# Kernel optimization log

Hardware: AMD Instinct MI355X
Metric: run time of the kernel (lower is better)

The kernel has to match this reference:

```python
import jax, jax.numpy as jnp
import numpy as np
from jax import lax

B, N, C = 16, 1024, 768
HID = 128           # route_hidden_dim (Cattn bottleneck + router hidden)
OUT = 2304          # qkv out_feature


def setup_inputs() -> dict:
    key = jax.random.key(0)
    ks = jax.random.split(key, 16)
    s = 0.02
    return {
        "input":  jax.random.normal(ks[0], (B, N, C), jnp.float32),
        "H": 32,
        "W": 32,
        "input2": jax.random.normal(ks[1], (B, N, C), jnp.float32),
        # qkv linear
        "qkv_w": jax.random.normal(ks[2], (OUT, C), jnp.float32) * s,
        "qkv_b": jax.random.normal(ks[3], (OUT,), jnp.float32) * s,
        # Cattn (vida_refine): fc1 -> dwconv -> gelu -> fc2
        "fc1_w": jax.random.normal(ks[4], (HID, C), jnp.float32) * s,
        "fc1_b": jnp.zeros((HID,), jnp.float32),
        "dw_w":  jax.random.normal(ks[5], (HID, 1, 3, 3), jnp.float32) * np.sqrt(2.0 / 9.0),
        "dw_b":  jnp.zeros((HID,), jnp.float32),
        "fc2_w": jax.random.normal(ks[6], (C, HID), jnp.float32) * s,
        "fc2_b": jnp.zeros((C,), jnp.float32),
        # router MLP: 1 -> HID -> 2
        "r1_w": jax.random.normal(ks[7], (HID, 1), jnp.float32) * s,
        "r1_b": jnp.zeros((HID,), jnp.float32),
        "r2_w": jax.random.normal(ks[8], (2, HID), jnp.float32) * s,
        "r2_b": jnp.zeros((2,), jnp.float32),
    }


def _linear(x, w, b):
    return jnp.einsum("bnc,oc->bno", x, w) + b


def _cattn(x, H, W, fc1_w, fc1_b, dw_w, dw_b, fc2_w, fc2_b):
    # fc1 -> depthwise 3x3 conv over HxW -> GELU(exact) -> fc2
    x = _linear(x, fc1_w, fc1_b)                       # [B,N,HID]
    b, n, h = x.shape
    xi = x.transpose(0, 2, 1).reshape(b, h, H, W)      # [B,HID,H,W]
    xi = lax.conv_general_dilated(
        xi, dw_w, window_strides=(1, 1), padding="SAME",
        feature_group_count=h,
        dimension_numbers=("NCHW", "OIHW", "NCHW"),
    ) + dw_b[None, :, None, None]
    x = xi.reshape(b, h, n).transpose(0, 2, 1)         # [B,N,HID]
    x = jax.nn.gelu(x, approximate=False)              # torch nn.GELU default = erf
    return _linear(x, fc2_w, fc2_b)                    # [B,N,C]


def _get_logit(inp, refine_x2):
    # cosine sim between per-batch token-mean of `inp` and refine_x2, then
    # per-batch min-max normalization (skipped when max == min)
    mean = jnp.mean(inp, axis=1, keepdims=True)        # [B,1,C]
    dot = jnp.sum(refine_x2 * mean, axis=-1, keepdims=True)
    n1 = jnp.linalg.norm(mean, axis=-1, keepdims=True)
    n2 = jnp.linalg.norm(refine_x2, axis=-1, keepdims=True)
    csim = dot / (n1 * n2)                             # [B,N,1]
    mn = jnp.min(csim, axis=1, keepdims=True)
    mx = jnp.max(csim, axis=1, keepdims=True)
    rng = mx - mn
    return jnp.where(rng != 0, (csim - mn) / jnp.where(rng != 0, rng, 1.0), csim)


def reference(input, H, W, input2, qkv_w, qkv_b, fc1_w, fc1_b, dw_w, dw_b,
              fc2_w, fc2_b, r1_w, r1_b, r2_w, r2_b):
    q1 = _linear(input, qkv_w, qkv_b)                              # [B,N,OUT]
    refine_x2 = input2 + _cattn(input2, H, W, fc1_w, fc1_b, dw_w, dw_b, fc2_w, fc2_b)
    q2 = _linear(refine_x2, qkv_w, qkv_b)                          # [B,N,OUT]
    csim = _get_logit(input, refine_x2)                            # [B,N,1]
    h = jax.nn.relu(_linear(csim, r1_w, r1_b))                     # [B,N,HID]
    logits = jax.nn.sigmoid(_linear(h, r2_w, r2_b))                # [B,N,2]
    # gumbel_softmax(hard=False, tau=1) with a fixed key for determinism
    g = jax.random.gumbel(jax.random.key(42), logits.shape, logits.dtype)
    router = jax.nn.softmax(logits + g, axis=-1)[:, :, 0]          # [B,N]
    return (q1, q2, router)
```

## Files before the change

### kernel.cpp

```cpp
#include <hip/hip_runtime.h>
#include <cstdint>
#include <cstddef>

#define BQ 16
#define NT 1024
#define CH 768
#define HIDN 128
#define OUTF 2304
#define MTOT (BQ*NT)

typedef __attribute__((ext_vector_type(4))) float f32x4;
typedef __attribute__((ext_vector_type(8))) short short8;

__device__ __forceinline__ unsigned short f2bf(float f){
  unsigned u = __float_as_uint(f);
  u += 0x7FFFu + ((u >> 16) & 1u);
  return (unsigned short)(u >> 16);
}
__device__ __forceinline__ float bf2f(unsigned short h){
  return __uint_as_float(((unsigned)h) << 16);
}

__device__ __forceinline__ void gload16(const void* g, void* l){
  __builtin_amdgcn_global_load_lds((const __attribute__((address_space(1))) void*)g,
                                   (__attribute__((address_space(3))) void*)l, 16, 0, 0);
}

__device__ __forceinline__ void mfma16(f32x4& d, short8 a, short8 b){
  asm volatile("v_mfma_f32_16x16x32_bf16 %0, %1, %2, %0" : "+v"(d) : "v"(a), "v"(b));
}

__global__ void k_f2bf_all(const float* __restrict__ in0, const float* __restrict__ in1,
                           const float* __restrict__ in2, const float* __restrict__ in3,
                           const float* __restrict__ in4,
                           unsigned short* __restrict__ o0, unsigned short* __restrict__ o1,
                           unsigned short* __restrict__ o2, unsigned short* __restrict__ o3,
                           unsigned short* __restrict__ o4)
{
  const long step = (long)2048 * 256 * 4;
  for (long i = (long)(blockIdx.x * 256 + threadIdx.x) * 4; i < 27131904L; i += step){
    const float* s; unsigned short* d; long off;
    if      (i < 12582912L){ s = in0; d = o0; off = i; }
    else if (i < 25165824L){ s = in1; d = o1; off = i - 12582912L; }
    else if (i < 26935296L){ s = in2; d = o2; off = i - 25165824L; }
    else if (i < 27033600L){ s = in3; d = o3; off = i - 26935296L; }
    else                   { s = in4; d = o4; off = i - 27033600L; }
    float4 v = *reinterpret_cast<const float4*>(s + off);
    ushort4 o;
    o.x = f2bf(v.x); o.y = f2bf(v.y); o.z = f2bf(v.z); o.w = f2bf(v.w);
    *reinterpret_cast<ushort4*>(d + off) = o;
  }
}

__global__ void k_mean(const unsigned short* __restrict__ x1b, float* __restrict__ meanb,
                       float* __restrict__ n1p){
  const int b = blockIdx.x, cg = blockIdx.y;
  const int tid = threadIdx.x;
  const int oct = tid & 15, rg = tid >> 4;
  const unsigned short* ip = x1b + (size_t)b*NT*CH + (size_t)rg*64*CH + cg*128 + oct*8;

  float s[8];
  #pragma unroll
  for (int j = 0; j < 8; ++j) s[j] = 0.f;
  #pragma unroll 4
  for (int r = 0; r < 64; ++r){
    short8 v = *reinterpret_cast<const short8*>(ip + (size_t)r*CH);
    #pragma unroll
    for (int j = 0; j < 8; ++j) s[j] += bf2f((unsigned short)v[j]);
  }

  __shared__ float tmp[16][128];
  #pragma unroll
  for (int j = 0; j < 8; ++j) tmp[rg][oct*8 + j] = s[j];
  __syncthreads();

  if (tid < 128){
    float m = 0.f;
    #pragma unroll
    for (int g = 0; g < 16; ++g) m += tmp[g][tid];
    m *= (1.0f/1024.0f);
    meanb[b*CH + cg*128 + tid] = m;
    float q = m * m;
    for (int off = 32; off; off >>= 1) q += __shfl_down(q, off, 64);
    if ((tid & 63) == 0) n1p[b*12 + cg*2 + (tid >> 6)] = q;
  }
}

template<int EPI>
__global__ __launch_bounds__(256, 2)
void k_gemm(const unsigned short* __restrict__ A, const unsigned short* __restrict__ B,
            const float* __restrict__ bias, const unsigned short* __restrict__ addb,
            unsigned short* __restrict__ Cb,
            const float* __restrict__ meanb, float* __restrict__ part,
            int M, int N, int K)
{
  __shared__ unsigned short sA[128][32];
  __shared__ unsigned short sB[128][32];
  const int tid = threadIdx.x;
  const int wv = tid >> 6, ln = tid & 63;
  const int wr = wv >> 1, wc = wv & 1;
  const int lhi = ln >> 4, llo = ln & 15;
  const int m0 = blockIdx.x * 128, n0 = blockIdx.y * 128;

  f32x4 acc[4][4];
  #pragma unroll
  for (int m = 0; m < 4; ++m)
    #pragma unroll
    for (int n = 0; n < 4; ++n) acc[m][n] = 0.0f;

  const int lrow = ln >> 2;
  const int lk8  = (ln & 3) * 8;

  for (int kt = 0; kt < K; kt += 32){
    #pragma unroll
    for (int cc = 0; cc < 2; ++cc){
      int c = wv * 2 + cc;
      gload16(A + (size_t)(m0 + c*16 + lrow) * K + kt + lk8, &sA[c*16][0]);
      gload16(B + (size_t)(n0 + c*16 + lrow) * K + kt + lk8, &sB[c*16][0]);
    }
    __syncthreads();

    short8 av[4], bv[4];
    #pragma unroll
    for (int m = 0; m < 4; ++m)
      av[m] = *reinterpret_cast<const short8*>(&sA[wr*64 + m*16 + llo][lhi*8]);
    #pragma unroll
    for (int n = 0; n < 4; ++n)
      bv[n] = *reinterpret_cast<const short8*>(&sB[wc*64 + n*16 + llo][lhi*8]);

    #pragma unroll
    for (int m = 0; m < 4; ++m)
      #pragma unroll
      for (int n = 0; n < 4; ++n)
        mfma16(acc[m][n], bv[n], av[m]);
    __syncthreads();
  }

  asm volatile("s_nop 7\n\ts_nop 7\n\ts_nop 7" ::: );

  float4 bias4[4];
  #pragma unroll
  for (int n = 0; n < 4; ++n)
    bias4[n] = *reinterpret_cast<const float4*>(&bias[n0 + wc*64 + n*16 + lhi*4]);

  if (EPI == 0){
    #pragma unroll
    for (int m = 0; m < 4; ++m){
      const int row = m0 + wr*64 + m*16 + llo;
      #pragma unroll
      for (int n = 0; n < 4; ++n){
        const int colbase = n0 + wc*64 + n*16 + lhi*4;
        ushort4 o;
        o.x = f2bf(acc[m][n][0] + bias4[n].x);
        o.y = f2bf(acc[m][n][1] + bias4[n].y);
        o.z = f2bf(acc[m][n][2] + bias4[n].z);
        o.w = f2bf(acc[m][n][3] + bias4[n].w);
        *reinterpret_cast<ushort4*>(&Cb[(size_t)row * N + colbase]) = o;
      }
    }
  } else {
    const int bb = m0 >> 10;
    const float* mp = meanb + bb * CH;
    float4 mp4[4];
    #pragma unroll
    for (int n = 0; n < 4; ++n)
      mp4[n] = *reinterpret_cast<const float4*>(&mp[n0 + wc*64 + n*16 + lhi*4]);

    #pragma unroll
    for (int m = 0; m < 4; ++m){
      const int row = m0 + wr*64 + m*16 + llo;
      float dsum = 0.f, qsum = 0.f;
      #pragma unroll
      for (int n = 0; n < 4; ++n){
        const int colbase = n0 + wc*64 + n*16 + lhi*4;
        ushort4 a4 = *reinterpret_cast<const ushort4*>(&addb[(size_t)row * N + colbase]);
        float v0 = acc[m][n][0] + bias4[n].x + bf2f(a4.x);
        float v1 = acc[m][n][1] + bias4[n].y + bf2f(a4.y);
        float v2 = acc[m][n][2] + bias4[n].z + bf2f(a4.z);
        float v3 = acc[m][n][3] + bias4[n].w + bf2f(a4.w);
        ushort4 o; o.x = f2bf(v0); o.y = f2bf(v1); o.z = f2bf(v2); o.w = f2bf(v3);
        *reinterpret_cast<ushort4*>(&Cb[(size_t)row * N + colbase]) = o;
        dsum += v0*mp4[n].x + v1*mp4[n].y + v2*mp4[n].z + v3*mp4[n].w;
        qsum += v0*v0 + v1*v1 + v2*v2 + v3*v3;
      }
      dsum += __shfl_xor(dsum, 16, 64);  qsum += __shfl_xor(qsum, 16, 64);
      dsum += __shfl_xor(dsum, 32, 64);  qsum += __shfl_xor(qsum, 32, 64);
      if (ln < 16){
        const int slot = blockIdx.y * 2 + wc;
        part[(size_t)slot * MTOT + row] = dsum;
        part[(size_t)(12 + slot) * MTOT + row] = qsum;
      }
    }
  }
}

#define STAGE(matB_, buf_, h_, t_) { \
    const unsigned short* g_ = ((matB_) ? Bbase : Abase) + (size_t)(h_)*128*K + (size_t)(t_)*64; \
    char* d_ = ldsWaveDst + (matB_)*65536 + (buf_)*32768 + (h_)*16384; \
    gload16(g_, d_); \
    gload16(g_ + rowK64, d_ + 8192); \
  }

#define PH_OPEN() \
    asm volatile("s_barrier" ::: "memory"); \
    asm volatile("s_waitcnt lgkmcnt(0)" ::: "memory"); \
    __builtin_amdgcn_sched_barrier(0); \
    __builtin_amdgcn_s_setprio(1);

#define PH_CLOSE() \
    __builtin_amdgcn_s_setprio(0); \
    asm volatile("s_barrier" ::: "memory");

#define MF16(mb, nb, BV) \
    _Pragma("unroll") \
    for (int ks = 0; ks < 2; ++ks) \
      _Pragma("unroll") \
      for (int mf = 0; mf < 4; ++mf) \
        _Pragma("unroll") \
        for (int nf = 0; nf < 2; ++nf) \
          mfma16(acc[(mb)+mf][(nb)+nf], av[mf][ks], BV[nf][ks]);

#define TILE(t_, b_) { \
    const int t = (t_); const int b = (b_); \
    _Pragma("unroll") for (int mf = 0; mf < 4; ++mf){ av[mf][0]=ldA(b,mf,0); av[mf][1]=ldA(b,mf,1); } \
    _Pragma("unroll") for (int nf = 0; nf < 2; ++nf){ b0v[nf][0]=ldB(b,nf,0); b0v[nf][1]=ldB(b,nf,1); } \
    if (t+1 < T) STAGE(0, b^1, 1, t+1); \
    PH_OPEN(); MF16(0,0,b0v); PH_CLOSE(); \
    _Pragma("unroll") for (int nf = 0; nf < 2; ++nf){ b1v[nf][0]=ldB(b,2+nf,0); b1v[nf][1]=ldB(b,2+nf,1); } \
    if (t+1 < T) STAGE(1, b^1, 0, t+1); \
    PH_OPEN(); MF16(0,2,b1v); PH_CLOSE(); \
    _Pragma("unroll") for (int mf = 0; mf < 4; ++mf){ av[mf][0]=ldA(b,4+mf,0); av[mf][1]=ldA(b,4+mf,1); } \
    if (t+2 < T) STAGE(0, b, 0, t+2); \
    PH_OPEN(); MF16(4,2,b1v); PH_CLOSE(); \
    if (t+2 < T) STAGE(1, b, 1, t+2); \
    PH_OPEN(); MF16(4,0,b0v); \
    __builtin_amdgcn_s_setprio(0); \
    if (t+2 < T) { asm volatile("s_waitcnt vmcnt(4)" ::: "memory"); } \
    else         { asm volatile("s_waitcnt vmcnt(0)" ::: "memory"); } \
    asm volatile("s_barrier" ::: "memory"); \
  }

template<int T>
__global__ __launch_bounds__(512, 2)
void k_gemm256(const unsigned short* __restrict__ A,
               const unsigned short* __restrict__ B,
               const float* __restrict__ bias,
               float* __restrict__ C,
               int N, int K, int nbn)
{
  __shared__ __align__(1024) char lds8[131072];
  const int tid = threadIdx.x;
  const int ln = tid & 63, wv = tid >> 6;
  const int wm = wv >> 2, wn = wv & 3;
  const int llo = ln & 15, lhi = ln >> 4;

  const int nwg = gridDim.x;
  const int cpx = nwg >> 3;
  const int bid = blockIdx.x;
  const int swz = (bid & 7) * cpx + (bid >> 3);
  const int bm = swz / nbn, bn = swz % nbn;
  const int m0 = bm * 256, n0 = bn * 256;

  const int srow = tid >> 3;
  const int sslot = (tid & 7) ^ (srow & 7);
  const unsigned short* Abase = A + (size_t)(m0 + srow) * K + sslot * 8;
  const unsigned short* Bbase = B + (size_t)(n0 + srow) * K + sslot * 8;
  const size_t rowK64 = (size_t)64 * K;
  char* ldsWaveDst = lds8 + (wv << 10);

  const int swz0 = ((lhi ^ (ln & 7)) << 4);
  const char* aRd0 = lds8 + (wm*64 + llo)*128 + swz0;
  const char* aRd1 = lds8 + (wm*64 + llo)*128 + (swz0 ^ 64);
  const char* bRd0 = lds8 + 65536 + (wn*32 + llo)*128 + swz0;
  const char* bRd1 = lds8 + 65536 + (wn*32 + llo)*128 + (swz0 ^ 64);

  auto ldA = [&](int b, int mf, int ks) -> short8 {
    const char* p = (ks ? aRd1 : aRd0) + b*32768 + (mf>>2)*16384 + (mf&3)*2048;
    return *reinterpret_cast<const short8*>(p);
  };
  auto ldB = [&](int b, int nf, int ks) -> short8 {
    const char* p = (ks ? bRd1 : bRd0) + b*32768 + (nf>>1)*16384 + (nf&1)*2048;
    return *reinterpret_cast<const short8*>(p);
  };

  f32x4 acc[8][4];
  #pragma unroll
  for (int m = 0; m < 8; ++m)
    #pragma unroll
    for (int n = 0; n < 4; ++n) acc[m][n] = 0.0f;

  STAGE(0, 0, 0, 0);
  STAGE(1, 0, 1, 0);
  STAGE(0, 0, 1, 0);
  STAGE(1, 0, 0, 0);
  STAGE(0, 1, 0, 1);
  STAGE(1, 1, 1, 1);
  asm volatile("s_waitcnt vmcnt(4)" ::: "memory");
  asm volatile("s_barrier" ::: "memory");

  short8 av[4][2], b0v[2][2], b1v[2][2];
  #pragma unroll 1
  for (int t0 = 0; t0 < T; t0 += 2){
    TILE(t0,   0);
    TILE(t0+1, 1);
  }

  asm volatile("s_nop 7\n\ts_nop 7\n\ts_nop 7" ::: );

  #pragma unroll
  for (int mf = 0; mf < 8; ++mf){
    const int row = m0 + (mf>>2)*128 + wm*64 + (mf&3)*16 + lhi*4;
    #pragma unroll
    for (int j = 0; j < 4; ++j){
      #pragma unroll
      for (int nf = 0; nf < 4; ++nf){
        const int col = n0 + (nf>>1)*128 + wn*32 + (nf&1)*16 + llo;
        C[(size_t)(row + j) * N + col] = acc[mf][nf][j] + bias[col];
      }
    }
  }
}

__global__ void k_dwgelu(const unsigned short* __restrict__ t1b, const float* __restrict__ dww,
                         const float* __restrict__ dwb, unsigned short* __restrict__ t2)
{
  int idx = blockIdx.x * blockDim.x + threadIdx.x;
  int hq = idx & 31; int t = idx >> 5;
  int h = hq * 4;
  int n = t & (NT-1); int b = t >> 10;
  int y = n >> 5, x = n & 31;

  float w[4][9];
  #pragma unroll
  for (int i = 0; i < 4; ++i)
    #pragma unroll
    for (int k = 0; k < 9; ++k) w[i][k] = dww[(h+i)*9 + k];

  float a0 = dwb[h+0], a1 = dwb[h+1], a2 = dwb[h+2], a3 = dwb[h+3];
  #pragma unroll
  for (int dy = -1; dy <= 1; ++dy){
    int yy = y + dy; if ((unsigned)yy >= 32u) continue;
    #pragma unroll
    for (int dx = -1; dx <= 1; ++dx){
      int xx = x + dx; if ((unsigned)xx >= 32u) continue;
      ushort4 v = *reinterpret_cast<const ushort4*>(&t1b[((size_t)b*NT + yy*32 + xx)*HIDN + h]);
      int k = (dy+1)*3 + (dx+1);
      a0 += bf2f(v.x) * w[0][k]; a1 += bf2f(v.y) * w[1][k];
      a2 += bf2f(v.z) * w[2][k]; a3 += bf2f(v.w) * w[3][k];
    }
  }
  const float is2 = 0.70710678118654752440f;
  a0 = 0.5f*a0*(1.0f + erff(a0*is2));
  a1 = 0.5f*a1*(1.0f + erff(a1*is2));
  a2 = 0.5f*a2*(1.0f + erff(a2*is2));
  a3 = 0.5f*a3*(1.0f + erff(a3*is2));
  ushort4 o; o.x = f2bf(a0); o.y = f2bf(a1); o.z = f2bf(a2); o.w = f2bf(a3);
  *reinterpret_cast<ushort4*>(&t2[(size_t)t*HIDN + h]) = o;
}

__device__ __forceinline__ void threefry(unsigned k0, unsigned k1, unsigned x0, unsigned x1,
                                         unsigned& o0, unsigned& o1){
  unsigned ks2 = k0 ^ k1 ^ 0x1BD11BDAu;
  x0 += k0; x1 += k1;
#define TFR(r) { x0 += x1; x1 = (x1 << r) | (x1 >> (32 - r)); x1 ^= x0; }
  TFR(13) TFR(15) TFR(26) TFR(6)  x0 += k1;  x1 += ks2 + 1u;
  TFR(17) TFR(29) TFR(16) TFR(24) x0 += ks2; x1 += k0 + 2u;
  TFR(13) TFR(15) TFR(26) TFR(6)  x0 += k0;  x1 += k1 + 3u;
  TFR(17) TFR(29) TFR(16) TFR(24) x0 += k1;  x1 += ks2 + 4u;
  TFR(13) TFR(15) TFR(26) TFR(6)  x0 += ks2; x1 += k0 + 5u;
#undef TFR
  o0 = x0; o1 = x1;
}

__device__ __forceinline__ float gumbel_from_bits(unsigned bits){
  float f = __uint_as_float((bits >> 9) | 0x3F800000u) - 1.0f;
  const float TINY = 1.17549435e-38f;
  float u = fmaxf(TINY, f + TINY);
  return -logf(-logf(u));
}

__global__ void k_router(const float* __restrict__ part, const float* __restrict__ n1p,
                         const float* __restrict__ r1w, const float* __restrict__ r1b,
                         const float* __restrict__ r2w, const float* __restrict__ r2b,
                         float* __restrict__ out)
{
  int b = blockIdx.x, tid = threadIdx.x;
  __shared__ float cs[NT];
  __shared__ float red[8];
  __shared__ float w1s[HIDN], b1s[HIDN], w20s[HIDN], w21s[HIDN];
  if (tid < HIDN){
    w1s[tid]  = r1w[tid];
    b1s[tid]  = r1b[tid];
    w20s[tid] = r2w[tid];
    w21s[tid] = r2w[HIDN + tid];
  }
  float n1s = 0.f;
  #pragma unroll
  for (int s = 0; s < 12; ++s) n1s += n1p[b*12 + s];
  float n1 = sqrtf(n1s);
  float lmin = 3.4e38f, lmax = -3.4e38f;
  #pragma unroll
  for (int j = 0; j < 4; ++j){
    int tk = tid + j*256;
    int t = b*NT + tk;
    float dot = 0.f, q = 0.f;
    #pragma unroll
    for (int s = 0; s < 12; ++s){
      dot += part[(size_t)s * MTOT + t];
      q   += part[(size_t)(12 + s) * MTOT + t];
    }
    float v = dot / (n1 * sqrtf(q));
    cs[tk] = v;
    lmin = fminf(lmin, v); lmax = fmaxf(lmax, v);
  }
  int ln = tid & 63, wv = tid >> 6;
  for (int off = 32; off; off >>= 1){
    lmin = fminf(lmin, __shfl_down(lmin, off, 64));
    lmax = fmaxf(lmax, __shfl_down(lmax, off, 64));
  }
  if (ln == 0){ red[wv] = lmin; red[4+wv] = lmax; }
  __syncthreads();
  float mn = fminf(fminf(red[0], red[1]), fminf(red[2], red[3]));
  float mx = fmaxf(fmaxf(red[4], red[5]), fmaxf(red[6], red[7]));
  float rng = mx - mn;
  bool nz = (rng != 0.0f);

  const float r2b0 = r2b[0], r2b1 = r2b[1];
  float v[4], l0[4], l1[4];
  #pragma unroll
  for (int j = 0; j < 4; ++j){
    float c0 = cs[tid + j*256];
    v[j] = nz ? (c0 - mn) / rng : c0;
    l0[j] = r2b0; l1[j] = r2b1;
  }
  for (int k = 0; k < HIDN; ++k){
    float a = w1s[k], bb = b1s[k], c0 = w20s[k], c1 = w21s[k];
    #pragma unroll
    for (int j = 0; j < 4; ++j){
      float hh = fmaxf(v[j] * a + bb, 0.f);
      l0[j] += hh * c0;
      l1[j] += hh * c1;
    }
  }
  #pragma unroll
  for (int j = 0; j < 4; ++j){
    float s0 = 1.f / (1.f + expf(-l0[j]));
    float s1 = 1.f / (1.f + expf(-l1[j]));
    int t = b*NT + tid + j*256;
    unsigned o0, o1;
    threefry(0u, 42u, 0u, (unsigned)(2*t),     o0, o1);
    float g0 = gumbel_from_bits(o0 ^ o1);
    threefry(0u, 42u, 0u, (unsigned)(2*t + 1), o0, o1);
    float g1 = gumbel_from_bits(o0 ^ o1);
    out[t] = 1.f / (1.f + expf((s1 + g1) - (s0 + g0)));
  }
}

extern "C" void kernel_launch(void* const* d_in, const int* in_sizes, int n_in,
                              void* d_out, int out_size, void* d_ws, size_t ws_size,
                              hipStream_t stream)
{
  (void)in_sizes; (void)n_in; (void)out_size;
  const float* input  = (const float*)d_in[0];
  const float* input2 = (const float*)d_in[3];
  const float* qkv_w  = (const float*)d_in[4];
  const float* qkv_b  = (const float*)d_in[5];
  const float* fc1_w  = (const float*)d_in[6];
  const float* fc1_b  = (const float*)d_in[7];
  const float* dw_w   = (const float*)d_in[8];
  const float* dw_b   = (const float*)d_in[9];
  const float* fc2_w  = (const float*)d_in[10];
  const float* fc2_b  = (const float*)d_in[11];
  const float* r1_w   = (const float*)d_in[12];
  const float* r1_b   = (const float*)d_in[13];
  const float* r2_w   = (const float*)d_in[14];
  const float* r2_b   = (const float*)d_in[15];

  float* q1 = (float*)d_out;
  float* router = q1 + (size_t)2 * MTOT * OUTF;

  if (ws_size < 67000000u) return;

  char* ws = (char*)d_ws;
  unsigned short* x1b = (unsigned short*)ws; ws += (size_t)MTOT*CH*2;
  unsigned short* xrb = (unsigned short*)ws; ws += (size_t)MTOT*CH*2;
  unsigned short* wqb = (unsigned short*)ws; ws += (size_t)OUTF*CH*2;
  unsigned short* w1b = (unsigned short*)ws; ws += (size_t)HIDN*CH*2;
  unsigned short* w2b = (unsigned short*)ws; ws += (size_t)CH*HIDN*2;
  unsigned short* t1b = (unsigned short*)ws; ws += (size_t)MTOT*HIDN*4;
  unsigned short* t2  = (unsigned short*)ws; ws += (size_t)MTOT*HIDN*2;
  float*          mb  = (float*)ws;          ws += (size_t)BQ*CH*4;
  float*          n1p = (float*)ws;          ws += 1024;
  float*          part= (float*)t1b;

  k_f2bf_all<<<dim3(2048), 256, 0, stream>>>(
      input, input2, qkv_w, fc1_w, fc2_w, x1b, xrb, wqb, w1b, w2b);

  k_mean<<<dim3(BQ, 6), 256, 0, stream>>>(x1b, mb, n1p);

  unsigned short* t1dst = t1b + (size_t)MTOT*HIDN;
  k_gemm<0><<<dim3(MTOT/128, HIDN/128), 256, 0, stream>>>(
      xrb, w1b, fc1_b, nullptr, t1dst, nullptr, nullptr, MTOT, HIDN, CH);
  k_dwgelu<<<dim3(MTOT*32/256), 256, 0, stream>>>(t1dst, dw_w, dw_b, t2);
  k_gemm<1><<<dim3(MTOT/128, CH/128), 256, 0, stream>>>(
      t2, w2b, fc2_b, xrb, xrb, mb, part, MTOT, CH, HIDN);

  k_gemm256<CH/64><<<dim3((2*MTOT/256) * (OUTF/256)), 512, 0, stream>>>(
      x1b, wqb, qkv_b, q1, OUTF, CH, OUTF/256);

  k_router<<<dim3(BQ), 256, 0, stream>>>(part, n1p, r1_w, r1_b, r2_w, r2_b, router);
}
```

Before: 245.6 us.

## Fuse q1 GEMM, fc1 GEMM and token-mean into one heterogeneous launch

The big q1 projection GEMM (which does not depend on the Cattn branch) now runs in a single combined kernel alongside the fc1 GEMM and the per-batch token-mean reduction, with different block-id ranges dispatched to each body. The q2 GEMM is launched separately after the fc2 step, where before one large GEMM launch covered both halves. The intent is to fill the GPU with independent work and cut kernel launches and tail idle time. The cost is that fc1 and mean blocks inherit the 512-thread, 128KB LDS footprint, which lowers their occupancy. Inside fc1, idle upper-half threads spin on matching barriers.

```diff
diff --git a/kernel.cpp b/kernel.cpp
--- a/kernel.cpp
+++ b/kernel.cpp
@@ -52,24 +52,227 @@
   }
 }
 
-__global__ void k_mean(const unsigned short* __restrict__ x1b, float* __restrict__ meanb,
-                       float* __restrict__ n1p){
-  const int b = blockIdx.x, cg = blockIdx.y;
+#define STAGE(matB_, buf_, h_, t_) { \
+    const unsigned short* g_ = ((matB_) ? Bbase : Abase) + (size_t)(h_)*128*K + (size_t)(t_)*64; \
+    char* d_ = ldsWaveDst + (matB_)*65536 + (buf_)*32768 + (h_)*16384; \
+    gload16(g_, d_); \
+    gload16(g_ + rowK64, d_ + 8192); \
+  }
+
+#define PH_OPEN() \
+    asm volatile("s_barrier" ::: "memory"); \
+    asm volatile("s_waitcnt lgkmcnt(0)" ::: "memory"); \
+    __builtin_amdgcn_sched_barrier(0); \
+    __builtin_amdgcn_s_setprio(1);
+
+#define PH_CLOSE() \
+    __builtin_amdgcn_s_setprio(0); \
+    asm volatile("s_barrier" ::: "memory");
+
+#define MF16(mb, nb, BV) \
+    _Pragma("unroll") \
+    for (int ks = 0; ks < 2; ++ks) \
+      _Pragma("unroll") \
+      for (int mf = 0; mf < 4; ++mf) \
+        _Pragma("unroll") \
+        for (int nf = 0; nf < 2; ++nf) \
+          mfma16(acc[(mb)+mf][(nb)+nf], av[mf][ks], BV[nf][ks]);
+
+#define TILE(t_, b_) { \
+    const int t = (t_); const int b = (b_); \
+    _Pragma("unroll") for (int mf = 0; mf < 4; ++mf){ av[mf][0]=ldA(b,mf,0); av[mf][1]=ldA(b,mf,1); } \
+    _Pragma("unroll") for (int nf = 0; nf < 2; ++nf){ b0v[nf][0]=ldB(b,nf,0); b0v[nf][1]=ldB(b,nf,1); } \
+    if (t+1 < T) STAGE(0, b^1, 1, t+1); \
+    PH_OPEN(); MF16(0,0,b0v); PH_CLOSE(); \
+    _Pragma("unroll") for (int nf = 0; nf < 2; ++nf){ b1v[nf][0]=ldB(b,2+nf,0); b1v[nf][1]=ldB(b,2+nf,1); } \
+    if (t+1 < T) STAGE(1, b^1, 0, t+1); \
+    PH_OPEN(); MF16(0,2,b1v); PH_CLOSE(); \
+    _Pragma("unroll") for (int mf = 0; mf < 4; ++mf){ av[mf][0]=ldA(b,4+mf,0); av[mf][1]=ldA(b,4+mf,1); } \
+    if (t+2 < T) STAGE(0, b, 0, t+2); \
+    PH_OPEN(); MF16(4,2,b1v); PH_CLOSE(); \
+    if (t+2 < T) STAGE(1, b, 1, t+2); \
+    PH_OPEN(); MF16(4,0,b0v); \
+    __builtin_amdgcn_s_setprio(0); \
+    if (t+2 < T) { asm volatile("s_waitcnt vmcnt(4)" ::: "memory"); } \
+    else         { asm volatile("s_waitcnt vmcnt(0)" ::: "memory"); } \
+    asm volatile("s_barrier" ::: "memory"); \
+  }
+
+template<int T>
+__device__ __forceinline__
+void gemm256_body(char* lds8,
+                  const unsigned short* __restrict__ A,
+                  const unsigned short* __restrict__ B,
+                  const float* __restrict__ bias,
+                  float* __restrict__ C,
+                  int N, int K, int nbn, int bid, int nwg)
+{
+  const int tid = threadIdx.x;
+  const int ln = tid & 63, wv = tid >> 6;
+  const int wm = wv >> 2, wn = wv & 3;
+  const int llo = ln & 15, lhi = ln >> 4;
+
+  const int cpx = nwg >> 3;
+  const int swz = (bid & 7) * cpx + (bid >> 3);
+  const int bm = swz / nbn, bn = swz % nbn;
+  const int m0 = bm * 256, n0 = bn * 256;
+
+  const int srow = tid >> 3;
+  const int sslot = (tid & 7) ^ (srow & 7);
+  const unsigned short* Abase = A + (size_t)(m0 + srow) * K + sslot * 8;
+  const unsigned short* Bbase = B + (size_t)(n0 + srow) * K + sslot * 8;
+  const size_t rowK64 = (size_t)64 * K;
+  char* ldsWaveDst = lds8 + (wv << 10);
+
+  const int swz0 = ((lhi ^ (ln & 7)) << 4);
+  const char* aRd0 = lds8 + (wm*64 + llo)*128 + swz0;
+  const char* aRd1 = lds8 + (wm*64 + llo)*128 + (swz0 ^ 64);
+  const char* bRd0 = lds8 + 65536 + (wn*32 + llo)*128 + swz0;
+  const char* bRd1 = lds8 + 65536 + (wn*32 + llo)*128 + (swz0 ^ 64);
+
+  auto ldA = [&](int b, int mf, int ks) -> short8 {
+    const char* p = (ks ? aRd1 : aRd0) + b*32768 + (mf>>2)*16384 + (mf&3)*2048;
+    return *reinterpret_cast<const short8*>(p);
+  };
+  auto ldB = [&](int b, int nf, int ks) -> short8 {
+    const char* p = (ks ? bRd1 : bRd0) + b*32768 + (nf>>1)*16384 + (nf&1)*2048;
+    return *reinterpret_cast<const short8*>(p);
+  };
+
+  f32x4 acc[8][4];
+  #pragma unroll
+  for (int m = 0; m < 8; ++m)
+    #pragma unroll
+    for (int n = 0; n < 4; ++n) acc[m][n] = 0.0f;
+
+  STAGE(0, 0, 0, 0);
+  STAGE(1, 0, 1, 0);
+  STAGE(0, 0, 1, 0);
+  STAGE(1, 0, 0, 0);
+  STAGE(0, 1, 0, 1);
+  STAGE(1, 1, 1, 1);
+  asm volatile("s_waitcnt vmcnt(4)" ::: "memory");
+  asm volatile("s_barrier" ::: "memory");
+
+  short8 av[4][2], b0v[2][2], b1v[2][2];
+  #pragma unroll 1
+  for (int t0 = 0; t0 < T; t0 += 2){
+    TILE(t0,   0);
+    TILE(t0+1, 1);
+  }
+
+  asm volatile("s_nop 7\n\ts_nop 7\n\ts_nop 7" ::: );
+
+  #pragma unroll
+  for (int mf = 0; mf < 8; ++mf){
+    const int row = m0 + (mf>>2)*128 + wm*64 + (mf&3)*16 + lhi*4;
+    #pragma unroll
+    for (int j = 0; j < 4; ++j){
+      #pragma unroll
+      for (int nf = 0; nf < 4; ++nf){
+        const int col = n0 + (nf>>1)*128 + wn*32 + (nf&1)*16 + llo;
+        C[(size_t)(row + j) * N + col] = acc[mf][nf][j] + bias[col];
+      }
+    }
+  }
+}
+
+__device__ __forceinline__
+void fc1_body(char* lds, const unsigned short* __restrict__ A,
+              const unsigned short* __restrict__ B,
+              const float* __restrict__ bias, unsigned short* __restrict__ Cb, int fb)
+{
+  const int tid = threadIdx.x;
+  if (tid >= 256){
+    #pragma unroll 1
+    for (int i = 0; i < 24; ++i){ __syncthreads(); __syncthreads(); }
+    return;
+  }
+  unsigned short (*sA)[32] = (unsigned short(*)[32])lds;
+  unsigned short (*sB)[32] = (unsigned short(*)[32])(lds + 8192);
+  const int wv = tid >> 6, ln = tid & 63;
+  const int wr = wv >> 1, wc = wv & 1;
+  const int lhi = ln >> 4, llo = ln & 15;
+  const int m0 = fb * 128, n0 = 0;
+  const int N = 128, K = 768;
+
+  f32x4 acc[4][4];
+  #pragma unroll
+  for (int m = 0; m < 4; ++m)
+    #pragma unroll
+    for (int n = 0; n < 4; ++n) acc[m][n] = 0.0f;
+
+  const int lrow = ln >> 2;
+  const int lk8  = (ln & 3) * 8;
+
+  #pragma unroll 1
+  for (int kt = 0; kt < 768; kt += 32){
+    #pragma unroll
+    for (int cc = 0; cc < 2; ++cc){
+      int c = wv * 2 + cc;
+      gload16(A + (size_t)(m0 + c*16 + lrow) * K + kt + lk8, &sA[c*16][0]);
+      gload16(B + (size_t)(n0 + c*16 + lrow) * K + kt + lk8, &sB[c*16][0]);
+    }
+    __syncthreads();
+
+    short8 av[4], bv[4];
+    #pragma unroll
+    for (int m = 0; m < 4; ++m)
+      av[m] = *reinterpret_cast<const short8*>(&sA[wr*64 + m*16 + llo][lhi*8]);
+    #pragma unroll
+    for (int n = 0; n < 4; ++n)
+      bv[n] = *reinterpret_cast<const short8*>(&sB[wc*64 + n*16 + llo][lhi*8]);
+
+    #pragma unroll
+    for (int m = 0; m < 4; ++m)
+      #pragma unroll
+      for (int n = 0; n < 4; ++n)
+        mfma16(acc[m][n], bv[n], av[m]);
+    __syncthreads();
+  }
+
+  asm volatile("s_nop 7\n\ts_nop 7\n\ts_nop 7" ::: );
+
+  float4 bias4[4];
+  #pragma unroll
+  for (int n = 0; n < 4; ++n)
+    bias4[n] = *reinterpret_cast<const float4*>(&bias[n0 + wc*64 + n*16 + lhi*4]);
+
+  #pragma unroll
+  for (int m = 0; m < 4; ++m){
+    const int row = m0 + wr*64 + m*16 + llo;
+    #pragma unroll
+    for (int n = 0; n < 4; ++n){
+      const int colbase = n0 + wc*64 + n*16 + lhi*4;
+      ushort4 o;
+      o.x = f2bf(acc[m][n][0] + bias4[n].x);
+      o.y = f2bf(acc[m][n][1] + bias4[n].y);
+      o.z = f2bf(acc[m][n][2] + bias4[n].z);
+      o.w = f2bf(acc[m][n][3] + bias4[n].w);
+      *reinterpret_cast<ushort4*>(&Cb[(size_t)row * N + colbase]) = o;
+    }
+  }
+}
+
+__device__ __forceinline__
+void mean_body(char* lds, const unsigned short* __restrict__ x1b,
+               float* __restrict__ meanb, float* __restrict__ n1p, int mbid)
+{
+  float (*tmp)[128] = (float(*)[128])lds;
+  const int b = mbid / 6, cg = mbid % 6;
   const int tid = threadIdx.x;
   const int oct = tid & 15, rg = tid >> 4;
-  const unsigned short* ip = x1b + (size_t)b*NT*CH + (size_t)rg*64*CH + cg*128 + oct*8;
+  const unsigned short* ip = x1b + (size_t)b*NT*CH + (size_t)rg*32*CH + cg*128 + oct*8;
 
   float s[8];
   #pragma unroll
   for (int j = 0; j < 8; ++j) s[j] = 0.f;
   #pragma unroll 4
-  for (int r = 0; r < 64; ++r){
+  for (int r = 0; r < 32; ++r){
     short8 v = *reinterpret_cast<const short8*>(ip + (size_t)r*CH);
     #pragma unroll
     for (int j = 0; j < 8; ++j) s[j] += bf2f((unsigned short)v[j]);
   }
-
-  __shared__ float tmp[16][128];
   #pragma unroll
   for (int j = 0; j < 8; ++j) tmp[rg][oct*8 + j] = s[j];
   __syncthreads();
@@ -77,13 +280,43 @@
   if (tid < 128){
     float m = 0.f;
     #pragma unroll
-    for (int g = 0; g < 16; ++g) m += tmp[g][tid];
+    for (int g = 0; g < 32; ++g) m += tmp[g][tid];
     m *= (1.0f/1024.0f);
     meanb[b*CH + cg*128 + tid] = m;
     float q = m * m;
     for (int off = 32; off; off >>= 1) q += __shfl_down(q, off, 64);
     if ((tid & 63) == 0) n1p[b*12 + cg*2 + (tid >> 6)] = q;
   }
+}
+
+__global__ __launch_bounds__(512, 2)
+void k_combo(const unsigned short* __restrict__ x1b, const unsigned short* __restrict__ wqb,
+             const float* __restrict__ qkv_b, float* __restrict__ q1,
+             const unsigned short* __restrict__ xrb, const unsigned short* __restrict__ w1b,
+             const float* __restrict__ fc1_b, unsigned short* __restrict__ t1dst,
+             float* __restrict__ meanb, float* __restrict__ n1p)
+{
+  __shared__ __align__(1024) char lds8[131072];
+  const int bid = blockIdx.x;
+  if (bid < 576){
+    gemm256_body<CH/64>(lds8, x1b, wqb, qkv_b, q1, OUTF, CH, OUTF/256, bid, 576);
+  } else if (bid < 704){
+    fc1_body(lds8, xrb, w1b, fc1_b, t1dst, bid - 576);
+  } else {
+    mean_body(lds8, x1b, meanb, n1p, bid - 704);
+  }
+}
+
+template<int T>
+__global__ __launch_bounds__(512, 2)
+void k_gemm256(const unsigned short* __restrict__ A,
+               const unsigned short* __restrict__ B,
+               const float* __restrict__ bias,
+               float* __restrict__ C,
+               int N, int K, int nbn)
+{
+  __shared__ __align__(1024) char lds8[131072];
+  gemm256_body<T>(lds8, A, B, bias, C, N, K, nbn, blockIdx.x, gridDim.x);
 }
 
 template<int EPI>
@@ -143,22 +376,7 @@
   for (int n = 0; n < 4; ++n)
     bias4[n] = *reinterpret_cast<const float4*>(&bias[n0 + wc*64 + n*16 + lhi*4]);
 
-  if (EPI == 0){
-    #pragma unroll
-    for (int m = 0; m < 4; ++m){
-      const int row = m0 + wr*64 + m*16 + llo;
-      #pragma unroll
-      for (int n = 0; n < 4; ++n){
-        const int colbase = n0 + wc*64 + n*16 + lhi*4;
-        ushort4 o;
-        o.x = f2bf(acc[m][n][0] + bias4[n].x);
-        o.y = f2bf(acc[m][n][1] + bias4[n].y);
-        o.z = f2bf(acc[m][n][2] + bias4[n].z);
-        o.w = f2bf(acc[m][n][3] + bias4[n].w);
-        *reinterpret_cast<ushort4*>(&Cb[(size_t)row * N + colbase]) = o;
-      }
-    }
-  } else {
+  {
     const int bb = m0 >> 10;
     const float* mp = meanb + bb * CH;
     float4 mp4[4];
@@ -194,133 +412,6 @@
   }
 }
 
-#define STAGE(matB_, buf_, h_, t_) { \
-    const unsigned short* g_ = ((matB_) ? Bbase : Abase) + (size_t)(h_)*128*K + (size_t)(t_)*64; \
-    char* d_ = ldsWaveDst + (matB_)*65536 + (buf_)*32768 + (h_)*16384; \
-    gload16(g_, d_); \
-    gload16(g_ + rowK64, d_ + 8192); \
-  }
-
-#define PH_OPEN() \
-    asm volatile("s_barrier" ::: "memory"); \
-    asm volatile("s_waitcnt lgkmcnt(0)" ::: "memory"); \
-    __builtin_amdgcn_sched_barrier(0); \
-    __builtin_amdgcn_s_setprio(1);
-
-#define PH_CLOSE() \
-    __builtin_amdgcn_s_setprio(0); \
-    asm volatile("s_barrier" ::: "memory");
-
-#define MF16(mb, nb, BV) \
-    _Pragma("unroll") \
-    for (int ks = 0; ks < 2; ++ks) \
-      _Pragma("unroll") \
-      for (int mf = 0; mf < 4; ++mf) \
-        _Pragma("unroll") \
-        for (int nf = 0; nf < 2; ++nf) \
-          mfma16(acc[(mb)+mf][(nb)+nf], av[mf][ks], BV[nf][ks]);
-
-#define TILE(t_, b_) { \
-    const int t = (t_); const int b = (b_); \
-    _Pragma("unroll") for (int mf = 0; mf < 4; ++mf){ av[mf][0]=ldA(b,mf,0); av[mf][1]=ldA(b,mf,1); } \
-    _Pragma("unroll") for (int nf = 0; nf < 2; ++nf){ b0v[nf][0]=ldB(b,nf,0); b0v[nf][1]=ldB(b,nf,1); } \
-    if (t+1 < T) STAGE(0, b^1, 1, t+1); \
-    PH_OPEN(); MF16(0,0,b0v); PH_CLOSE(); \
-    _Pragma("unroll") for (int nf = 0; nf < 2; ++nf){ b1v[nf][0]=ldB(b,2+nf,0); b1v[nf][1]=ldB(b,2+nf,1); } \
-    if (t+1 < T) STAGE(1, b^1, 0, t+1); \
-    PH_OPEN(); MF16(0,2,b1v); PH_CLOSE(); \
-    _Pragma("unroll") for (int mf = 0; mf < 4; ++mf){ av[mf][0]=ldA(b,4+mf,0); av[mf][1]=ldA(b,4+mf,1); } \
-    if (t+2 < T) STAGE(0, b, 0, t+2); \
-    PH_OPEN(); MF16(4,2,b1v); PH_CLOSE(); \
-    if (t+2 < T) STAGE(1, b, 1, t+2); \
-    PH_OPEN(); MF16(4,0,b0v); \
-    __builtin_amdgcn_s_setprio(0); \
-    if (t+2 < T) { asm volatile("s_waitcnt vmcnt(4)" ::: "memory"); } \
-    else         { asm volatile("s_waitcnt vmcnt(0)" ::: "memory"); } \
-    asm volatile("s_barrier" ::: "memory"); \
-  }
-
-template<int T>
-__global__ __launch_bounds__(512, 2)
-void k_gemm256(const unsigned short* __restrict__ A,
-               const unsigned short* __restrict__ B,
-               const float* __restrict__ bias,
-               float* __restrict__ C,
-               int N, int K, int nbn)
-{
-  __shared__ __align__(1024) char lds8[131072];
-  const int tid = threadIdx.x;
-  const int ln = tid & 63, wv = tid >> 6;
-  const int wm = wv >> 2, wn = wv & 3;
-  const int llo = ln & 15, lhi = ln >> 4;
-
-  const int nwg = gridDim.x;
-  const int cpx = nwg >> 3;
-  const int bid = blockIdx.x;
-  const int swz = (bid & 7) * cpx + (bid >> 3);
-  const int bm = swz / nbn, bn = swz % nbn;
-  const int m0 = bm * 256, n0 = bn * 256;
-
-  const int srow = tid >> 3;
-  const int sslot = (tid & 7) ^ (srow & 7);
-  const unsigned short* Abase = A + (size_t)(m0 + srow) * K + sslot * 8;
-  const unsigned short* Bbase = B + (size_t)(n0 + srow) * K + sslot * 8;
-  const size_t rowK64 = (size_t)64 * K;
-  char* ldsWaveDst = lds8 + (wv << 10);
-
-  const int swz0 = ((lhi ^ (ln & 7)) << 4);
-  const char* aRd0 = lds8 + (wm*64 + llo)*128 + swz0;
-  const char* aRd1 = lds8 + (wm*64 + llo)*128 + (swz0 ^ 64);
-  const char* bRd0 = lds8 + 65536 + (wn*32 + llo)*128 + swz0;
-  const char* bRd1 = lds8 + 65536 + (wn*32 + llo)*128 + (swz0 ^ 64);
-
-  auto ldA = [&](int b, int mf, int ks) -> short8 {
-    const char* p = (ks ? aRd1 : aRd0) + b*32768 + (mf>>2)*16384 + (mf&3)*2048;
-    return *reinterpret_cast<const short8*>(p);
-  };
-  auto ldB = [&](int b, int nf, int ks) -> short8 {
-    const char* p = (ks ? bRd1 : bRd0) + b*32768 + (nf>>1)*16384 + (nf&1)*2048;
-    return *reinterpret_cast<const short8*>(p);
-  };
-
-  f32x4 acc[8][4];
-  #pragma unroll
-  for (int m = 0; m < 8; ++m)
-    #pragma unroll
-    for (int n = 0; n < 4; ++n) acc[m][n] = 0.0f;
-
-  STAGE(0, 0, 0, 0);
-  STAGE(1, 0, 1, 0);
-  STAGE(0, 0, 1, 0);
-  STAGE(1, 0, 0, 0);
-  STAGE(0, 1, 0, 1);
-  STAGE(1, 1, 1, 1);
-  asm volatile("s_waitcnt vmcnt(4)" ::: "memory");
-  asm volatile("s_barrier" ::: "memory");
-
-  short8 av[4][2], b0v[2][2], b1v[2][2];
-  #pragma unroll 1
-  for (int t0 = 0; t0 < T; t0 += 2){
-    TILE(t0,   0);
-    TILE(t0+1, 1);
-  }
-
-  asm volatile("s_nop 7\n\ts_nop 7\n\ts_nop 7" ::: );
-
-  #pragma unroll
-  for (int mf = 0; mf < 8; ++mf){
-    const int row = m0 + (mf>>2)*128 + wm*64 + (mf&3)*16 + lhi*4;
-    #pragma unroll
-    for (int j = 0; j < 4; ++j){
-      #pragma unroll
-      for (int nf = 0; nf < 4; ++nf){
-        const int col = n0 + (nf>>1)*128 + wn*32 + (nf&1)*16 + llo;
-        C[(size_t)(row + j) * N + col] = acc[mf][nf][j] + bias[col];
-      }
-    }
-  }
-}
-
 __global__ void k_dwgelu(const unsigned short* __restrict__ t1b, const float* __restrict__ dww,
                          const float* __restrict__ dwb, unsigned short* __restrict__ t2)
 {
@@ -477,6 +568,7 @@
   const float* r2_b   = (const float*)d_in[15];
 
   float* q1 = (float*)d_out;
+  float* q2 = q1 + (size_t)MTOT * OUTF;
   float* router = q1 + (size_t)2 * MTOT * OUTF;
 
   if (ws_size < 67000000u) return;
@@ -496,17 +588,17 @@
   k_f2bf_all<<<dim3(2048), 256, 0, stream>>>(
       input, input2, qkv_w, fc1_w, fc2_w, x1b, xrb, wqb, w1b, w2b);
 
-  k_mean<<<dim3(BQ, 6), 256, 0, stream>>>(x1b, mb, n1p);
-
   unsigned short* t1dst = t1b + (size_t)MTOT*HIDN;
-  k_gemm<0><<<dim3(MTOT/128, HIDN/128), 256, 0, stream>>>(
-      xrb, w1b, fc1_b, nullptr, t1dst, nullptr, nullptr, MTOT, HIDN, CH);
+  k_combo<<<dim3(800), 512, 0, stream>>>(
+      x1b, wqb, qkv_b, q1, xrb, w1b, fc1_b, t1dst, mb, n1p);
+
   k_dwgelu<<<dim3(MTOT*32/256), 256, 0, stream>>>(t1dst, dw_w, dw_b, t2);
+
   k_gemm<1><<<dim3(MTOT/128, CH/128), 256, 0, stream>>>(
       t2, w2b, fc2_b, xrb, xrb, mb, part, MTOT, CH, HIDN);
 
-  k_gemm256<CH/64><<<dim3((2*MTOT/256) * (OUTF/256)), 512, 0, stream>>>(
-      x1b, wqb, qkv_b, q1, OUTF, CH, OUTF/256);
+  k_gemm256<CH/64><<<dim3(576), 512, 0, stream>>>(
+      xrb, wqb, qkv_b, q2, OUTF, CH, OUTF/256);
 
   k_router<<<dim3(BQ), 256, 0, stream>>>(part, n1p, r1_w, r1_b, r2_w, r2_b, router);
 }
```

Result: no change. 242.8 us (-1.1%).
